# Kernel tuning notes

Measured on AMD Instinct MI355X. Metric: run time of the kernel, lower is better.

## Reference

```python
import jax, jax.numpy as jnp
import numpy as np

LN_EPS = 1e-12  # BERT LayerNorm eps


def _layernorm(x, g, b):
    mu = jnp.mean(x, axis=-1, keepdims=True)
    var = jnp.mean(jnp.square(x - mu), axis=-1, keepdims=True)
    return (x - mu) * jax.lax.rsqrt(var + LN_EPS) * g + b


def setup_inputs() -> dict:
    key = jax.random.key(0)
    B, M, D, H, dh, R, Ro, Rf, F = 4, 2048, 768, 12, 64, 32, 256, 256, 3072
    ks = iter(jax.random.split(key, 32))
    n = lambda shape, s=0.02: jax.random.normal(next(ks), shape, jnp.float32) * s
    return {
        'x': jax.random.normal(next(ks), (B, M, D), jnp.float32),
        'mask': jnp.zeros((B, M), jnp.float32),  # HF-style additive mask
        'Pq': n((H, D, R)), 'Vq': n((H, R, dh)), 'bq': n((1, H, 1, dh)),
        'Pk': n((H, D, R)), 'Vk': n((H, R, dh)), 'bk': n((1, H, 1, dh)),
        'Pv': n((H, D, R)), 'Vv': n((H, R, dh)), 'bv': n((1, H, 1, dh)),
        'Uo': n((D, Ro)), 'Vo': n((Ro, D)), 'bo_attn': jnp.zeros((D,), jnp.float32),
        'U1': n((D, Rf)), 'V1': n((Rf, F)), 'b1': jnp.zeros((F,), jnp.float32),
        'U2': n((F, Rf)), 'V2': n((Rf, D)), 'b2': jnp.zeros((D,), jnp.float32),
        'ln1_g': jnp.ones((D,), jnp.float32), 'ln1_b': jnp.zeros((D,), jnp.float32),
        'ln2_g': jnp.ones((D,), jnp.float32), 'ln2_b': jnp.zeros((D,), jnp.float32),
    }


def reference(x, mask, Pq, Vq, bq, Pk, Vk, bk, Pv, Vv, bv,
              Uo, Vo, bo_attn, U1, V1, b1, U2, V2, b2,
              ln1_g, ln1_b, ln2_g, ln2_b):
    B, M, D = x.shape
    H, dh = Pq.shape[0], Vq.shape[2]
    # low-rank per-head Q/K/V: x @ P (bhmr) then @ V (bhmd) + bias
    q = jnp.einsum('bhmr,hrd->bhmd', jnp.einsum('bmd,hdr->bhmr', x, Pq), Vq) + bq
    k = jnp.einsum('bhmr,hrd->bhmd', jnp.einsum('bmd,hdr->bhmr', x, Pk), Vk) + bk
    v = jnp.einsum('bhmr,hrd->bhmd', jnp.einsum('bmd,hdr->bhmr', x, Pv), Vv) + bv
    # attention (flash_svd_attention math: scaled dot-product + additive mask)
    scores = jnp.einsum('bhmd,bhnd->bhmn', q, k) / jnp.sqrt(jnp.float32(dh))
    scores = scores + mask[:, None, None, :]
    attn = jnp.einsum('bhmn,bhnd->bhmd', jax.nn.softmax(scores, axis=-1), v)
    attn = attn.transpose(0, 2, 1, 3).reshape(B, M, D)
    # low-rank output projection + residual + LN1
    x1 = _layernorm(x + (attn @ Uo) @ Vo + bo_attn, ln1_g, ln1_b)
    # low-rank FFN (BERT intermediate: exact GELU)
    mid = x1 @ U1
    y = (jax.nn.gelu(mid @ V1 + b1, approximate=False) @ U2) @ V2 + b2
    return _layernorm(x1 + y, ln2_g, ln2_b)
```

## Files before the change

### kernel.cpp

```cpp
#include <hip/hip_runtime.h>
#include <hip/hip_bf16.h>
#include <math.h>

typedef __hip_bfloat16 bf16;
typedef __attribute__((ext_vector_type(8))) short short8;
typedef __attribute__((ext_vector_type(4))) short short4v;
typedef __attribute__((ext_vector_type(4))) float f32x4;

#define C1F 0.18033688011112042f
#define LOG2E 1.44269504088896f

__device__ __forceinline__ float to_f(float x) { return x; }
__device__ __forceinline__ float to_f(bf16 x) { return __bfloat162float(x); }

template <typename T> __device__ __forceinline__ T from_f(float x);
template <> __device__ __forceinline__ float from_f<float>(float x) { return x; }
template <> __device__ __forceinline__ bf16 from_f<bf16>(float x) { return __float2bfloat16(x); }

__device__ __forceinline__ float gelu_exact(float x) {
    return 0.5f * x * (1.0f + erff(x * 0.70710678118654752f));
}

#define GLD_LDS16(g, l)                                               \
    __builtin_amdgcn_global_load_lds(                                 \
        (const __attribute__((address_space(1))) void*)(g),           \
        (__attribute__((address_space(3))) void*)(l), 16, 0, 0)

__global__ __launch_bounds__(256) void build_w_qkv_lds(const float* __restrict__ Pq,
                                                       const float* __restrict__ Vq,
                                                       const float* __restrict__ Pk,
                                                       const float* __restrict__ Vk,
                                                       const float* __restrict__ Pv,
                                                       const float* __restrict__ Vv,
                                                       bf16* __restrict__ Wt) {
    const int dt = blockIdx.x;
    const int h = blockIdx.y;
    const int which = blockIdx.z;
    const float* P = (which == 0) ? Pq : (which == 1) ? Pk : Pv;
    const float* V = (which == 0) ? Vq : (which == 1) ? Vk : Vv;
    const float scale = (which == 0) ? C1F : 1.0f;
    __shared__ __align__(16) float Ps[128][36];
    __shared__ __align__(16) float Vs[32][64];
    __shared__ __align__(16) unsigned int Ot[64][68];
    const int tid = threadIdx.x;

    const float* pbase = P + ((size_t)h * 768 + dt * 128) * 32;
#pragma unroll
    for (int i = 0; i < 4; i++) {
        int idx = tid + i * 256;
        float4 v4 = ((const float4*)pbase)[idx];
        *(float4*)&Ps[idx >> 3][(idx & 7) * 4] = v4;
    }
    const float* vbase = V + (size_t)h * 2048;
#pragma unroll
    for (int i = 0; i < 2; i++) {
        int idx = tid + i * 256;
        ((float4*)&Vs[0][0])[idx] = ((const float4*)vbase)[idx];
    }
    __syncthreads();

    const int e = tid & 63, w = tid >> 6;
    float vreg[32];
#pragma unroll
    for (int r = 0; r < 32; r++) vreg[r] = Vs[r][e];

#pragma unroll
    for (int dp = 0; dp < 16; dp++) {
        const int d0 = w * 32 + dp * 2;
        float a0 = 0.f, a1 = 0.f;
#pragma unroll
        for (int r4 = 0; r4 < 8; r4++) {
            float4 p0 = *(const float4*)&Ps[d0][r4 * 4];
            float4 p1 = *(const float4*)&Ps[d0 + 1][r4 * 4];
            a0 += p0.x * vreg[r4 * 4] + p0.y * vreg[r4 * 4 + 1] + p0.z * vreg[r4 * 4 + 2] + p0.w * vreg[r4 * 4 + 3];
            a1 += p1.x * vreg[r4 * 4] + p1.y * vreg[r4 * 4 + 1] + p1.z * vreg[r4 * 4 + 2] + p1.w * vreg[r4 * 4 + 3];
        }
        a0 *= scale;
        a1 *= scale;
        unsigned int lo = (unsigned int)(unsigned short)__builtin_bit_cast(short, from_f<bf16>(a0));
        unsigned int hi = (unsigned int)(unsigned short)__builtin_bit_cast(short, from_f<bf16>(a1));
        Ot[e][w * 16 + dp] = lo | (hi << 16);
    }
    __syncthreads();

    const int erow = tid >> 2, c0 = (tid & 3) * 16;
    bf16* dst = Wt + ((size_t)which * 768 + h * 64 + erow) * 768 + dt * 128 + c0 * 2;
    *(uint4*)(dst) = *(const uint4*)&Ot[erow][c0];
    *(uint4*)(dst + 8) = *(const uint4*)&Ot[erow][c0 + 4];
    *(uint4*)(dst + 16) = *(const uint4*)&Ot[erow][c0 + 8];
    *(uint4*)(dst + 24) = *(const uint4*)&Ot[erow][c0 + 12];
}

__device__ __forceinline__ void ct_tile(const float* in, bf16* out, int R, int Cc,
                                        int r0, int c0, int tx, int ty) {
    __shared__ float t[32][33];
#pragma unroll
    for (int i = 0; i < 4; i++)
        t[ty + i * 8][tx] = in[(size_t)(r0 + ty + i * 8) * Cc + c0 + tx];
    __syncthreads();
#pragma unroll
    for (int i = 0; i < 4; i++)
        out[(size_t)(c0 + ty + i * 8) * R + r0 + tx] = from_f<bf16>(t[tx][ty + i * 8]);
}

__global__ __launch_bounds__(256) void cast_transpose_batch(const float* __restrict__ U1,
                                                            const float* __restrict__ V1,
                                                            const float* __restrict__ U2,
                                                            const float* __restrict__ V2,
                                                            const float* __restrict__ Vo,
                                                            bf16* __restrict__ U1t,
                                                            bf16* __restrict__ V1t,
                                                            bf16* __restrict__ U2t,
                                                            bf16* __restrict__ V2t,
                                                            bf16* __restrict__ Vot) {
    int t = blockIdx.x;
    const float* in;
    bf16* out;
    int R, Cc;
    if (t < 192) { in = U1; out = U1t; R = 768; Cc = 256; }
    else if (t < 960) { t -= 192; in = V1; out = V1t; R = 256; Cc = 3072; }
    else if (t < 1728) { t -= 960; in = U2; out = U2t; R = 3072; Cc = 256; }
    else if (t < 1920) { t -= 1728; in = V2; out = V2t; R = 256; Cc = 768; }
    else { t -= 1920; in = Vo; out = Vot; R = 256; Cc = 768; }
    const int tpr = Cc >> 5;
    ct_tile(in, out, R, Cc, (t / tpr) * 32, (t % tpr) * 32,
            threadIdx.x & 31, threadIdx.x >> 5);
}

__global__ __launch_bounds__(256) void cast_f32_bf16_dual(const float* __restrict__ a,
                                                          bf16* __restrict__ oa, int n4a,
                                                          const float* __restrict__ bsrc,
                                                          bf16* __restrict__ ob, int n4b) {
    int t = blockIdx.x * 256 + threadIdx.x;
    const float* in;
    bf16* out;
    int i;
    if (t < n4a) { in = a; out = oa; i = t; }
    else if (t < n4a + n4b) { in = bsrc; out = ob; i = t - n4a; }
    else return;
    float4 v = ((const float4*)in)[i];
    bf16 tmp[4] = {from_f<bf16>(v.x), from_f<bf16>(v.y), from_f<bf16>(v.z), from_f<bf16>(v.w)};
    ((short4v*)out)[i] = *(short4v*)tmp;
}

__global__ __launch_bounds__(256) void pack_bias_mask(const float* __restrict__ bq,
                                                      const float* __restrict__ bk,
                                                      const float* __restrict__ bv,
                                                      const float* __restrict__ mask,
                                                      float* __restrict__ bias_out,
                                                      float* __restrict__ mask2) {
    int t = blockIdx.x * 256 + threadIdx.x;
    if (t < 768) {
        bias_out[t] = bq[t] * C1F;
        bias_out[768 + t] = bk[t];
        bias_out[1536 + t] = bv[t];
    }
    int m = t - 768;
    if (m >= 0 && m < 8192) mask2[m] = mask[m] * LOG2E;
}

template <typename TOUT, int EPI>
__global__ __launch_bounds__(256) void gemm_mfma(const bf16* __restrict__ A,
                                                 const bf16* __restrict__ Bt,
                                                 const float* __restrict__ bias,
                                                 TOUT* __restrict__ C,
                                                 int M, int N, int K) {
    __shared__ __align__(16) bf16 As[128 * 32];
    __shared__ __align__(16) bf16 Bs[128 * 32];
    const int tid = threadIdx.x;
    const int w = tid >> 6, lane = tid & 63;
    const int l = lane & 15, quad = lane >> 4;
    const int wm = w >> 1, wn = w & 1;
    const int m0 = blockIdx.x * 128, n0 = blockIdx.y * 128;

    const int r_in = lane >> 2;
    const int slot = lane & 3;
    const int rA0 = 2 * w * 16 + r_in, rA1 = rA0 + 16;
    const int q0 = slot ^ ((rA0 >> 1) & 3);
    const int q1 = slot ^ ((rA1 >> 1) & 3);
    const bf16* a0 = A + (size_t)(m0 + rA0) * K + q0 * 8;
    const bf16* a1 = A + (size_t)(m0 + rA1) * K + q1 * 8;
    const bf16* b0 = Bt + (size_t)(n0 + rA0) * K + q0 * 8;
    const bf16* b1 = Bt + (size_t)(n0 + rA1) * K + q1 * 8;
    bf16* lA0 = As + 2 * w * 512;
    bf16* lA1 = lA0 + 512;
    bf16* lB0 = Bs + 2 * w * 512;
    bf16* lB1 = lB0 + 512;

    const int swz = (quad ^ ((l >> 1) & 3)) * 8;
    f32x4 acc[4][4] = {};

    for (int k0 = 0; k0 < K; k0 += 32) {
        GLD_LDS16(a0 + k0, lA0);
        GLD_LDS16(a1 + k0, lA1);
        GLD_LDS16(b0 + k0, lB0);
        GLD_LDS16(b1 + k0, lB1);
        __syncthreads();
        short8 af[4], bfr[4];
#pragma unroll
        for (int mt = 0; mt < 4; mt++)
            af[mt] = *(const short8*)&As[(wm * 64 + mt * 16 + l) * 32 + swz];
#pragma unroll
        for (int nt = 0; nt < 4; nt++)
            bfr[nt] = *(const short8*)&Bs[(wn * 64 + nt * 16 + l) * 32 + swz];
#pragma unroll
        for (int mt = 0; mt < 4; mt++)
#pragma unroll
            for (int nt = 0; nt < 4; nt++)
                acc[mt][nt] = __builtin_amdgcn_mfma_f32_16x16x32_bf16(af[mt], bfr[nt], acc[mt][nt], 0, 0, 0);
        __syncthreads();
    }

    float bs[4];
#pragma unroll
    for (int nt = 0; nt < 4; nt++)
        bs[nt] = bias ? bias[n0 + wn * 64 + nt * 16 + l] : 0.f;
#pragma unroll
    for (int mt = 0; mt < 4; mt++) {
#pragma unroll
        for (int nt = 0; nt < 4; nt++) {
            const int col = n0 + wn * 64 + nt * 16 + l;
#pragma unroll
            for (int r = 0; r < 4; r++) {
                const int row = m0 + wm * 64 + mt * 16 + quad * 4 + r;
                float val = acc[mt][nt][r] + bs[nt];
                if (EPI == 1) val = gelu_exact(val);
                C[(size_t)row * N + col] = from_f<TOUT>(val);
            }
        }
    }
}

template <typename TOUT, int EPI>
__global__ __launch_bounds__(256) void gemm_mfma64(const bf16* __restrict__ A,
                                                   const bf16* __restrict__ Bt,
                                                   const float* __restrict__ bias,
                                                   TOUT* __restrict__ C,
                                                   int M, int N, int K) {
    __shared__ __align__(16) bf16 As[64 * 32];
    __shared__ __align__(16) bf16 Bs[64 * 32];
    const int tid = threadIdx.x;
    const int w = tid >> 6, lane = tid & 63;
    const int l = lane & 15, quad = lane >> 4;
    const int wm = w >> 1, wn = w & 1;
    const int m0 = blockIdx.x * 64, n0 = blockIdx.y * 64;

    const int cid = tid;
    const int srow = cid >> 2, slot = cid & 3;
    const int gq = slot ^ ((srow >> 1) & 3);
    const bf16* ag = A + (size_t)(m0 + srow) * K + gq * 8;
    const bf16* bg = Bt + (size_t)(n0 + srow) * K + gq * 8;
    bf16* lA = As + w * 512;
    bf16* lB = Bs + w * 512;

    f32x4 acc[2][2] = {};

    for (int k0 = 0; k0 < K; k0 += 32) {
        GLD_LDS16(ag + k0, lA);
        GLD_LDS16(bg + k0, lB);
        __syncthreads();
        short8 af[2], bfr[2];
#pragma unroll
        for (int mt = 0; mt < 2; mt++) {
            const int row = wm * 32 + mt * 16 + l;
            af[mt] = *(const short8*)&As[row * 32 + (quad ^ ((row >> 1) & 3)) * 8];
        }
#pragma unroll
        for (int nt = 0; nt < 2; nt++) {
            const int row = wn * 32 + nt * 16 + l;
            bfr[nt] = *(const short8*)&Bs[row * 32 + (quad ^ ((row >> 1) & 3)) * 8];
        }
#pragma unroll
        for (int mt = 0; mt < 2; mt++)
#pragma unroll
            for (int nt = 0; nt < 2; nt++)
                acc[mt][nt] = __builtin_amdgcn_mfma_f32_16x16x32_bf16(af[mt], bfr[nt], acc[mt][nt], 0, 0, 0);
        __syncthreads();
    }

#pragma unroll
    for (int mt = 0; mt < 2; mt++) {
#pragma unroll
        for (int nt = 0; nt < 2; nt++) {
            const int col = n0 + wn * 32 + nt * 16 + l;
            const float bsv = bias ? bias[col] : 0.f;
#pragma unroll
            for (int r = 0; r < 4; r++) {
                const int row = m0 + wm * 32 + mt * 16 + quad * 4 + r;
                float val = acc[mt][nt][r] + bsv;
                if (EPI == 1) val = gelu_exact(val);
                C[(size_t)row * N + col] = from_f<TOUT>(val);
            }
        }
    }
}

__global__ __launch_bounds__(256) void transpose_v(const bf16* __restrict__ qkv,
                                                   bf16* __restrict__ vt) {
    __shared__ __align__(16) bf16 t[64][72];
    const int m0 = blockIdx.x * 64;
    const int h = blockIdx.y;
    const int tid = threadIdx.x;
    const int r = tid >> 2, c0 = (tid & 3) * 16;
    {
        const size_t g = (size_t)(m0 + r) * 2304 + 1536 + h * 64 + c0;
        *(short8*)&t[r][c0] = *(const short8*)(qkv + g);
        *(short8*)&t[r][c0 + 8] = *(const short8*)(qkv + g + 8);
    }
    __syncthreads();
    const int b = m0 >> 11, mm = m0 & 2047;
    const int e = tid >> 2, mi0 = (tid & 3) * 16;
    bf16 tmp[16];
#pragma unroll
    for (int j = 0; j < 16; j++) tmp[j] = t[mi0 + j][e];
    bf16* dst = vt + (((size_t)b * 12 + h) * 64 + e) * 2048 + mm + mi0;
    *(short8*)dst = *(short8*)&tmp[0];
    *(short8*)(dst + 8) = *(short8*)&tmp[8];
}

__global__ __launch_bounds__(256, 4) void flash_attn_mfma(const bf16* __restrict__ qkv,
                                                          const bf16* __restrict__ vt,
                                                          const float* __restrict__ mask2,
                                                          bf16* __restrict__ opart0,
                                                          bf16* __restrict__ opart1,
                                                          float* __restrict__ lpart) {
    const int qt = blockIdx.x, h = blockIdx.y;
    const int b = blockIdx.z >> 1, kh = blockIdx.z & 1;
    const int tid = threadIdx.x;
    const int w = tid >> 6, lane = tid & 63;
    const int l = lane & 15, quad = lane >> 4;

    __shared__ __align__(16) bf16 Ks[2][64 * 64];
    __shared__ __align__(16) bf16 Vs[2][64 * 64];
    __shared__ __align__(16) bf16 Ps[4 * 16 * 64];

    short8 qf[2][2];
#pragma unroll
    for (int mt = 0; mt < 2; mt++) {
        const int qrow = qt * 128 + w * 32 + mt * 16 + l;
        const bf16* qp = qkv + ((size_t)b * 2048 + qrow) * 2304 + h * 64 + quad * 8;
        qf[mt][0] = *(const short8*)qp;
        qf[mt][1] = *(const short8*)(qp + 32);
    }

    short8 ones;
#pragma unroll
    for (int i = 0; i < 8; i++) ones[i] = (short)0x3F80;

    f32x4 of[2][4] = {};
    f32x4 lacc[2] = {};
    bf16* Pw = Ps + w * 1024;

    const int kc0 = kh * 1024;
    int ldst[2];
    const bf16* kg[2];
    const bf16* vg[2];
#pragma unroll
    for (int i = 0; i < 2; i++) {
        const int cid = (w * 2 + i) * 64 + lane;
        const int row = cid >> 3, slot = cid & 7;
        const int gq = slot ^ (row & 7);
        ldst[i] = cid * 8;
        kg[i] = qkv + ((size_t)b * 2048 + kc0 + row) * 2304 + 768 + h * 64 + gq * 8;
        vg[i] = vt + (((size_t)b * 12 + h) * 64 + row) * 2048 + kc0 + gq * 8;
    }
    const float* mp = mask2 + (size_t)b * 2048 + kc0 + quad * 4;

    auto stage = [&](int buf) {
#pragma unroll
        for (int i = 0; i < 2; i++) {
            GLD_LDS16(kg[i], &Ks[buf][ldst[i]]);
            GLD_LDS16(vg[i], &Vs[buf][ldst[i]]);
            kg[i] += 64 * 2304;
            vg[i] += 64;
        }
    };

    int cur = 0;
    stage(0);

#pragma unroll 2
    for (int it = 0; it < 16; it++) {
        __syncthreads();
        float4 mrow[4];
#pragma unroll
        for (int nt = 0; nt < 4; nt++) mrow[nt] = *(const float4*)(mp + nt * 16);
        mp += 64;
        if (it < 15) stage(cur ^ 1);

        const bf16* Kc = Ks[cur];
        const bf16* Vc = Vs[cur];

        f32x4 st[2][4];
#pragma unroll
        for (int nt = 0; nt < 4; nt++) {
            const int rb = (nt * 16 + l) * 64;
            short8 kf0 = *(const short8*)&Kc[rb + ((quad) ^ (l & 7)) * 8];
            short8 kf1 = *(const short8*)&Kc[rb + ((4 + quad) ^ (l & 7)) * 8];
#pragma unroll
            for (int mt = 0; mt < 2; mt++) {
                f32x4 a = {mrow[nt].x, mrow[nt].y, mrow[nt].z, mrow[nt].w};
                a = __builtin_amdgcn_mfma_f32_16x16x32_bf16(kf0, qf[mt][0], a, 0, 0, 0);
                a = __builtin_amdgcn_mfma_f32_16x16x32_bf16(kf1, qf[mt][1], a, 0, 0, 0);
                st[mt][nt] = a;
            }
        }

        short8 pa[2][2];
#pragma unroll
        for (int mt = 0; mt < 2; mt++) {
#pragma unroll
            for (int nt = 0; nt < 4; nt++) {
                float p0 = exp2f(st[mt][nt][0]);
                float p1 = exp2f(st[mt][nt][1]);
                float p2 = exp2f(st[mt][nt][2]);
                float p3 = exp2f(st[mt][nt][3]);
                unsigned d0 = __builtin_amdgcn_perm(__builtin_bit_cast(unsigned, p1),
                                                    __builtin_bit_cast(unsigned, p0), 0x07060302u);
                unsigned d1 = __builtin_amdgcn_perm(__builtin_bit_cast(unsigned, p3),
                                                    __builtin_bit_cast(unsigned, p2), 0x07060302u);
                const int slot8 = (2 * nt + (quad >> 1)) ^ (l & 7);
                uint2 u = {d0, d1};
                *(uint2*)&Pw[l * 64 + slot8 * 8 + (quad & 1) * 4] = u;
            }
#pragma unroll
            for (int ks = 0; ks < 2; ks++)
                pa[mt][ks] = *(const short8*)&Pw[l * 64 + ((ks * 4 + quad) ^ (l & 7)) * 8];
        }

#pragma unroll
        for (int mt = 0; mt < 2; mt++) {
            lacc[mt] = __builtin_amdgcn_mfma_f32_16x16x32_bf16(pa[mt][0], ones, lacc[mt], 0, 0, 0);
            lacc[mt] = __builtin_amdgcn_mfma_f32_16x16x32_bf16(pa[mt][1], ones, lacc[mt], 0, 0, 0);
        }

#pragma unroll
        for (int nt = 0; nt < 4; nt++) {
            const int rb = (nt * 16 + l) * 64;
            short8 vf0 = *(const short8*)&Vc[rb + ((quad) ^ (l & 7)) * 8];
            short8 vf1 = *(const short8*)&Vc[rb + ((4 + quad) ^ (l & 7)) * 8];
#pragma unroll
            for (int mt = 0; mt < 2; mt++) {
                of[mt][nt] = __builtin_amdgcn_mfma_f32_16x16x32_bf16(pa[mt][0], vf0, of[mt][nt], 0, 0, 0);
                of[mt][nt] = __builtin_amdgcn_mfma_f32_16x16x32_bf16(pa[mt][1], vf1, of[mt][nt], 0, 0, 0);
            }
        }
        cur ^= 1;
    }

#pragma unroll
    for (int mt = 0; mt < 2; mt++) {
        if (l == 0) {
#pragma unroll
            for (int r = 0; r < 4; r++)
                lpart[(((size_t)kh * 4 + b) * 12 + h) * 2048 + qt * 128 + w * 32 + mt * 16 + quad * 4 + r] =
                    lacc[mt][r];
        }
    }

    bf16* op = kh ? opart1 : opart0;
#pragma unroll
    for (int mt = 0; mt < 2; mt++) {
#pragma unroll
        for (int r = 0; r < 4; r++) {
            const int row = qt * 128 + w * 32 + mt * 16 + quad * 4 + r;
#pragma unroll
            for (int nt = 0; nt < 4; nt++)
                op[((size_t)b * 2048 + row) * 768 + h * 64 + nt * 16 + l] =
                    from_f<bf16>(of[mt][nt][r]);
        }
    }
}

__global__ __launch_bounds__(256) void attn_combine(const bf16* __restrict__ o0,
                                                    const bf16* __restrict__ o1,
                                                    const float* __restrict__ lp,
                                                    bf16* __restrict__ outp) {
    const int t = blockIdx.x * 256 + threadIdx.x;
    const int col4 = t % 192;
    const int row = t / 192;
    const int b = row >> 11, m = row & 2047;
    const int h = col4 >> 4;
    const float l0 = lp[((size_t)b * 12 + h) * 2048 + m];
    const float l1 = lp[((size_t)(4 + b) * 12 + h) * 2048 + m];
    const float iv = 1.f / (l0 + l1);
    short4v a = ((const short4v*)o0)[t];
    short4v c = ((const short4v*)o1)[t];
    bf16 r[4];
#pragma unroll
    for (int i = 0; i < 4; i++) {
        float f = to_f(__builtin_bit_cast(bf16, a[i])) + to_f(__builtin_bit_cast(bf16, c[i]));
        r[i] = from_f<bf16>(f * iv);
    }
    ((short4v*)outp)[t] = *(short4v*)r;
}

template <typename TIN, typename TADD, typename TOUT>
__global__ __launch_bounds__(256) void ln_kernel(const TIN* __restrict__ base,
                                                 const TADD* __restrict__ add,
                                                 const float* __restrict__ gamma,
                                                 const float* __restrict__ beta,
                                                 TOUT* __restrict__ out) {
    const int row = blockIdx.x;
    const int tid = threadIdx.x;
    __shared__ float red[4];
    const size_t o = (size_t)row * 768;
    float v[3];
#pragma unroll
    for (int i = 0; i < 3; i++) {
        int d = tid + i * 256;
        v[i] = to_f(base[o + d]) + to_f(add[o + d]);
    }
    float s = v[0] + v[1] + v[2];
#pragma unroll
    for (int off = 32; off > 0; off >>= 1) s += __shfl_down(s, off, 64);
    const int wave = tid >> 6, lane = tid & 63;
    if (lane == 0) red[wave] = s;
    __syncthreads();
    float mu = (red[0] + red[1] + red[2] + red[3]) * (1.0f / 768.0f);
    float d0 = v[0] - mu, d1 = v[1] - mu, d2 = v[2] - mu;
    float sq = d0 * d0 + d1 * d1 + d2 * d2;
    __syncthreads();
#pragma unroll
    for (int off = 32; off > 0; off >>= 1) sq += __shfl_down(sq, off, 64);
    if (lane == 0) red[wave] = sq;
    __syncthreads();
    float var = (red[0] + red[1] + red[2] + red[3]) * (1.0f / 768.0f);
    float rs = rsqrtf(var + 1e-12f);
#pragma unroll
    for (int i = 0; i < 3; i++) {
        int d = tid + i * 256;
        float y = (v[i] - mu) * rs * gamma[d] + beta[d];
        out[o + d] = from_f<TOUT>(y);
    }
}

extern "C" void kernel_launch(void* const* d_in, const int* in_sizes, int n_in,
                              void* d_out, int out_size, void* d_ws, size_t ws_size,
                              hipStream_t stream) {
    const float* x    = (const float*)d_in[0];
    const float* mask = (const float*)d_in[1];
    const float* Pq = (const float*)d_in[2];
    const float* Vq = (const float*)d_in[3];
    const float* bq = (const float*)d_in[4];
    const float* Pk = (const float*)d_in[5];
    const float* Vk = (const float*)d_in[6];
    const float* bk = (const float*)d_in[7];
    const float* Pv = (const float*)d_in[8];
    const float* Vv = (const float*)d_in[9];
    const float* bv = (const float*)d_in[10];
    const float* Uo = (const float*)d_in[11];
    const float* Vo = (const float*)d_in[12];
    const float* bo = (const float*)d_in[13];
    const float* U1 = (const float*)d_in[14];
    const float* V1 = (const float*)d_in[15];
    const float* b1 = (const float*)d_in[16];
    const float* U2 = (const float*)d_in[17];
    const float* V2 = (const float*)d_in[18];
    const float* b2 = (const float*)d_in[19];
    const float* g1 = (const float*)d_in[20];
    const float* be1 = (const float*)d_in[21];
    const float* g2 = (const float*)d_in[22];
    const float* be2 = (const float*)d_in[23];

    char* p = (char*)d_ws;
    bf16* Wqkv_t = (bf16*)p;            p += (size_t)2304 * 768 * 2;
    bf16* Wo_t   = (bf16*)p;            p += (size_t)768 * 768 * 2;
    bf16* U1t    = (bf16*)p;            p += (size_t)256 * 768 * 2;
    bf16* V1t    = (bf16*)p;            p += (size_t)3072 * 256 * 2;
    bf16* U2t    = (bf16*)p;            p += (size_t)256 * 3072 * 2;
    bf16* V2t    = (bf16*)p;            p += (size_t)768 * 256 * 2;
    float* bias_qkv = (float*)p;        p += (size_t)2304 * 4;
    float* mask2 = (float*)p;           p += (size_t)8192 * 4;
    bf16* xb     = (bf16*)p;
    bf16* x1b    = xb;                  p += (size_t)8192 * 768 * 2;
    bf16* qkv    = (bf16*)p;
    bf16* gbuf   = qkv;                 p += (size_t)8192 * 2304 * 2;
    bf16* vtb    = (bf16*)p;            p += (size_t)8192 * 768 * 2;
    bf16* attnb  = (bf16*)p;
    bf16* t2     = attnb;               p += (size_t)8192 * 768 * 2;
    char* regR   = p;                   p += (size_t)8192 * 768 * 4;
    bf16* t1     = (bf16*)p;            p += (size_t)8192 * 256 * 2;
    bf16* Vot = (bf16*)regR;
    bf16* Uob = Vot + (size_t)768 * 256;
    bf16* opart1 = (bf16*)regR;
    float* lpart = (float*)(regR + (size_t)8192 * 768 * 2);
    bf16* y1b = (bf16*)regR;
    bf16* y2b = (bf16*)(regR + (size_t)8192 * 768 * 2);

    constexpr int N4_X = 8192 * 768 / 4;
    constexpr int N4_UO = 768 * 256 / 4;
    constexpr int CAST_BLOCKS = (N4_X + N4_UO + 255) / 256;
    build_w_qkv_lds<<<dim3(6, 12, 3), 256, 0, stream>>>(Pq, Vq, Pk, Vk, Pv, Vv, Wqkv_t);
    cast_transpose_batch<<<2112, 256, 0, stream>>>(U1, V1, U2, V2, Vo, U1t, V1t, U2t, V2t, Vot);
    cast_f32_bf16_dual<<<CAST_BLOCKS, 256, 0, stream>>>(x, xb, N4_X, Uo, Uob, N4_UO);
    pack_bias_mask<<<35, 256, 0, stream>>>(bq, bk, bv, mask, bias_qkv, mask2);
    gemm_mfma<bf16, 0><<<dim3(6, 6), 256, 0, stream>>>(Vot, Uob, nullptr, Wo_t, 768, 768, 256);

    gemm_mfma<bf16, 0><<<dim3(64, 18), 256, 0, stream>>>(xb, Wqkv_t, bias_qkv, qkv, 8192, 2304, 768);

    transpose_v<<<dim3(128, 12), 256, 0, stream>>>(qkv, vtb);

    flash_attn_mfma<<<dim3(16, 12, 8), 256, 0, stream>>>(qkv, vtb, mask2, attnb, opart1, lpart);
    attn_combine<<<6144, 256, 0, stream>>>(attnb, opart1, lpart, attnb);

    gemm_mfma<bf16, 0><<<dim3(64, 6), 256, 0, stream>>>(attnb, Wo_t, bo, y1b, 8192, 768, 768);

    ln_kernel<bf16, bf16, bf16><<<8192, 256, 0, stream>>>(xb, y1b, g1, be1, x1b);

    gemm_mfma64<bf16, 0><<<dim3(128, 4), 256, 0, stream>>>(x1b, U1t, nullptr, t1, 8192, 256, 768);

    gemm_mfma<bf16, 1><<<dim3(64, 24), 256, 0, stream>>>(t1, V1t, b1, gbuf, 8192, 3072, 256);

    gemm_mfma64<bf16, 0><<<dim3(128, 4), 256, 0, stream>>>(gbuf, U2t, nullptr, t2, 8192, 256, 3072);

    gemm_mfma<bf16, 0><<<dim3(64, 6), 256, 0, stream>>>(t2, V2t, b2, y2b, 8192, 768, 256);

    ln_kernel<bf16, bf16, float><<<8192, 256, 0, stream>>>(x1b, y2b, g2, be2, (float*)d_out);
}
```

Before: 420.2 us.

## Double-buffer LDS tiles in both MFMA GEMM kernels to overlap loads with compute

Both bf16 MFMA GEMM kernels now keep two LDS buffers for A and B. The next 32-wide K slice is issued via global_load_lds while MFMAs run on the current one, and the loop is unrolled by two. The aim is to hide global-to-LDS latency that the old single-buffer loop exposed by waiting on every slice before computing. It doubles LDS use per block, which may lower occupancy. It also assumes K is a multiple of 64, so a K=32 or other odd-multiple call would read past the slice and accumulate garbage.

Result: no change. 417.3 us (-0.7%).

```diff
diff --git a/kernel.cpp b/kernel.cpp
--- a/kernel.cpp
+++ b/kernel.cpp
@@ -165,8 +165,8 @@
                                                  const float* __restrict__ bias,
                                                  TOUT* __restrict__ C,
                                                  int M, int N, int K) {
-    __shared__ __align__(16) bf16 As[128 * 32];
-    __shared__ __align__(16) bf16 Bs[128 * 32];
+    __shared__ __align__(16) bf16 As[2][128 * 32];
+    __shared__ __align__(16) bf16 Bs[2][128 * 32];
     const int tid = threadIdx.x;
     const int w = tid >> 6, lane = tid & 63;
     const int l = lane & 15, quad = lane >> 4;
@@ -182,33 +182,41 @@
     const bf16* a1 = A + (size_t)(m0 + rA1) * K + q1 * 8;
     const bf16* b0 = Bt + (size_t)(n0 + rA0) * K + q0 * 8;
     const bf16* b1 = Bt + (size_t)(n0 + rA1) * K + q1 * 8;
-    bf16* lA0 = As + 2 * w * 512;
-    bf16* lA1 = lA0 + 512;
-    bf16* lB0 = Bs + 2 * w * 512;
-    bf16* lB1 = lB0 + 512;
+    const int lofs0 = 2 * w * 512;
+    const int lofs1 = lofs0 + 512;
 
     const int swz = (quad ^ ((l >> 1) & 3)) * 8;
     f32x4 acc[4][4] = {};
 
-    for (int k0 = 0; k0 < K; k0 += 32) {
-        GLD_LDS16(a0 + k0, lA0);
-        GLD_LDS16(a1 + k0, lA1);
-        GLD_LDS16(b0 + k0, lB0);
-        GLD_LDS16(b1 + k0, lB1);
-        __syncthreads();
+    auto stage = [&](int k0, int buf) {
+        GLD_LDS16(a0 + k0, &As[buf][lofs0]);
+        GLD_LDS16(a1 + k0, &As[buf][lofs1]);
+        GLD_LDS16(b0 + k0, &Bs[buf][lofs0]);
+        GLD_LDS16(b1 + k0, &Bs[buf][lofs1]);
+    };
+    auto compute = [&](int buf) {
         short8 af[4], bfr[4];
 #pragma unroll
         for (int mt = 0; mt < 4; mt++)
-            af[mt] = *(const short8*)&As[(wm * 64 + mt * 16 + l) * 32 + swz];
+            af[mt] = *(const short8*)&As[buf][(wm * 64 + mt * 16 + l) * 32 + swz];
 #pragma unroll
         for (int nt = 0; nt < 4; nt++)
-            bfr[nt] = *(const short8*)&Bs[(wn * 64 + nt * 16 + l) * 32 + swz];
+            bfr[nt] = *(const short8*)&Bs[buf][(wn * 64 + nt * 16 + l) * 32 + swz];
 #pragma unroll
         for (int mt = 0; mt < 4; mt++)
 #pragma unroll
             for (int nt = 0; nt < 4; nt++)
                 acc[mt][nt] = __builtin_amdgcn_mfma_f32_16x16x32_bf16(af[mt], bfr[nt], acc[mt][nt], 0, 0, 0);
+    };
+
+    stage(0, 0);
+    for (int k0 = 0; k0 < K; k0 += 64) {
         __syncthreads();
+        stage(k0 + 32, 1);
+        compute(0);
+        __syncthreads();
+        if (k0 + 64 < K) stage(k0 + 64, 0);
+        compute(1);
     }
 
     float bs[4];
@@ -237,45 +245,53 @@
                                                    const float* __restrict__ bias,
                                                    TOUT* __restrict__ C,
                                                    int M, int N, int K) {
-    __shared__ __align__(16) bf16 As[64 * 32];
-    __shared__ __align__(16) bf16 Bs[64 * 32];
+    __shared__ __align__(16) bf16 As[2][64 * 32];
+    __shared__ __align__(16) bf16 Bs[2][64 * 32];
     const int tid = threadIdx.x;
     const int w = tid >> 6, lane = tid & 63;
     const int l = lane & 15, quad = lane >> 4;
     const int wm = w >> 1, wn = w & 1;
     const int m0 = blockIdx.x * 64, n0 = blockIdx.y * 64;
 
-    const int cid = tid;
-    const int srow = cid >> 2, slot = cid & 3;
+    const int srow = tid >> 2, slot = tid & 3;
     const int gq = slot ^ ((srow >> 1) & 3);
     const bf16* ag = A + (size_t)(m0 + srow) * K + gq * 8;
     const bf16* bg = Bt + (size_t)(n0 + srow) * K + gq * 8;
-    bf16* lA = As + w * 512;
-    bf16* lB = Bs + w * 512;
+    const int lofs = w * 512;
 
     f32x4 acc[2][2] = {};
 
-    for (int k0 = 0; k0 < K; k0 += 32) {
-        GLD_LDS16(ag + k0, lA);
-        GLD_LDS16(bg + k0, lB);
-        __syncthreads();
+    auto stage = [&](int k0, int buf) {
+        GLD_LDS16(ag + k0, &As[buf][lofs]);
+        GLD_LDS16(bg + k0, &Bs[buf][lofs]);
+    };
+    auto compute = [&](int buf) {
         short8 af[2], bfr[2];
 #pragma unroll
         for (int mt = 0; mt < 2; mt++) {
             const int row = wm * 32 + mt * 16 + l;
-            af[mt] = *(const short8*)&As[row * 32 + (quad ^ ((row >> 1) & 3)) * 8];
+            af[mt] = *(const short8*)&As[buf][row * 32 + (quad ^ ((row >> 1) & 3)) * 8];
         }
 #pragma unroll
         for (int nt = 0; nt < 2; nt++) {
             const int row = wn * 32 + nt * 16 + l;
-            bfr[nt] = *(const short8*)&Bs[row * 32 + (quad ^ ((row >> 1) & 3)) * 8];
+            bfr[nt] = *(const short8*)&Bs[buf][row * 32 + (quad ^ ((row >> 1) & 3)) * 8];
         }
 #pragma unroll
         for (int mt = 0; mt < 2; mt++)
 #pragma unroll
             for (int nt = 0; nt < 2; nt++)
                 acc[mt][nt] = __builtin_amdgcn_mfma_f32_16x16x32_bf16(af[mt], bfr[nt], acc[mt][nt], 0, 0, 0);
+    };
+
+    stage(0, 0);
+    for (int k0 = 0; k0 < K; k0 += 64) {
         __syncthreads();
+        stage(k0 + 32, 1);
+        compute(0);
+        __syncthreads();
+        if (k0 + 64 < K) stage(k0 + 64, 0);
+        compute(1);
     }
 
 #pragma unroll
```
